# Performance work log

Hardware: AMD Instinct MI355X
Metric: run time of the kernel (lower is better)

The kernel has to match this reference:

```python
import math
import jax, jax.numpy as jnp
import numpy as np

B, T, C = 4, 2048, 1024
H = 16
D = C // H  # head dim = 64


def setup_inputs() -> dict:
    key = jax.random.key(0)
    ks = jax.random.split(key, 9)
    s = 0.02
    return {
        "x": jax.random.normal(ks[0], (B, T, C), dtype=jnp.float32),
        "Wq": jax.random.normal(ks[1], (C, C), dtype=jnp.float32) * s,
        "bq": jax.random.normal(ks[2], (C,), dtype=jnp.float32) * s,
        "Wk": jax.random.normal(ks[3], (C, C), dtype=jnp.float32) * s,
        "bk": jax.random.normal(ks[4], (C,), dtype=jnp.float32) * s,
        "Wv": jax.random.normal(ks[5], (C, C), dtype=jnp.float32) * s,
        "bv": jax.random.normal(ks[6], (C,), dtype=jnp.float32) * s,
        "Wo": jax.random.normal(ks[7], (C, C), dtype=jnp.float32) * s,
        "bo": jax.random.normal(ks[8], (C,), dtype=jnp.float32) * s,
    }


def reference(x, Wq, bq, Wk, bk, Wv, bv, Wo, bo):
    # Linear projections (torch Linear: x @ W.T + b), split into heads -> [B,H,T,D]
    def heads(y):
        return y.reshape(B, T, H, D).transpose(0, 2, 1, 3)

    q = heads(x @ Wq.T + bq)
    k = heads(x @ Wk.T + bk)
    v = heads(x @ Wv.T + bv)

    # Full [B,H,T,T] score matrix, scaled by 1/sqrt(D) (no mask, dropout=0 / eval)
    scores = jnp.einsum("bhqd,bhkd->bhqk", q, k) / math.sqrt(D)
    attn = jax.nn.softmax(scores, axis=-1)
    out = jnp.einsum("bhqk,bhkd->bhqd", attn, v)
    out = out.transpose(0, 2, 1, 3).reshape(B, T, C)
    return out @ Wo.T + bo
```

## Files before the change

kernel.cpp:

```cpp
#include <hip/hip_runtime.h>
#include <hip/hip_bf16.h>
#include <stdint.h>

#define Bb 4
#define Tt 2048
#define Cc 1024
#define Hh 16
#define Dd 64

using bf16x8 = __bf16 __attribute__((ext_vector_type(8)));
using f32x4  = float  __attribute__((ext_vector_type(4)));
using f32x16 = float  __attribute__((ext_vector_type(16)));
typedef unsigned short u16;
typedef unsigned int   u32;

#if defined(__has_builtin) && __has_builtin(__builtin_amdgcn_exp2f)
#define EXP2F(x) __builtin_amdgcn_exp2f(x)
#else
#define EXP2F(x) exp2f(x)
#endif

#if defined(__has_builtin) && __has_builtin(__builtin_amdgcn_permlane32_swap)
#define PERMLANE32_SWAP(a, b)                                          \
  do {                                                                 \
    auto _r = __builtin_amdgcn_permlane32_swap((a), (b), false, false);\
    (a) = _r[0]; (b) = _r[1];                                          \
  } while (0)
#else
#define PERMLANE32_SWAP(a, b) \
  asm volatile("v_permlane32_swap_b32 %0, %1" : "+v"(a), "+v"(b))
#endif

__device__ __forceinline__ u16 f32_to_bf16(float f) {
  union { float f; unsigned u; } v; v.f = f;
  unsigned r = v.u + 0x7fffu + ((v.u >> 16) & 1u);
  return (u16)(r >> 16);
}

__device__ __forceinline__ void gl2lds16(const u16* g, u16* l) {
  __builtin_amdgcn_global_load_lds(
      (const __attribute__((address_space(1))) u32*)g,
      (__attribute__((address_space(3))) u32*)l, 16, 0, 0);
}

__global__ void cast_f32_to_bf16(const float* __restrict__ in, u16* __restrict__ out, int n) {
  int i = (blockIdx.x * blockDim.x + threadIdx.x) * 4;
  if (i >= n) return;
  float4 v = *reinterpret_cast<const float4*>(in + i);
  ushort4 o;
  o.x = f32_to_bf16(v.x); o.y = f32_to_bf16(v.y);
  o.z = f32_to_bf16(v.z); o.w = f32_to_bf16(v.w);
  *reinterpret_cast<ushort4*>(out + i) = o;
}

__global__ void cast4_f32_to_bf16(const float* __restrict__ w0, const float* __restrict__ w1,
                                  const float* __restrict__ w2, const float* __restrict__ w3,
                                  u16* __restrict__ o0, u16* __restrict__ o1,
                                  u16* __restrict__ o2, u16* __restrict__ o3, int n) {
  const float* in; u16* out;
  switch (blockIdx.y) {
    case 0: in = w0; out = o0; break;
    case 1: in = w1; out = o1; break;
    case 2: in = w2; out = o2; break;
    default: in = w3; out = o3; break;
  }
  int i = (blockIdx.x * blockDim.x + threadIdx.x) * 4;
  if (i >= n) return;
  float4 v = *reinterpret_cast<const float4*>(in + i);
  ushort4 o;
  o.x = f32_to_bf16(v.x); o.y = f32_to_bf16(v.y);
  o.z = f32_to_bf16(v.z); o.w = f32_to_bf16(v.w);
  *reinterpret_cast<ushort4*>(out + i) = o;
}

__global__ __launch_bounds__(256, 2)
void gemm_qkv(const u16* __restrict__ A, const u16* __restrict__ Bqkv,
              const float* __restrict__ bq, const float* __restrict__ bk,
              const float* __restrict__ bv,
              u16* __restrict__ qout, u16* __restrict__ kout, u16* __restrict__ vtout,
              float qscl)
{
  constexpr int K = Cc, BK = 32, LDT = 136;
  __shared__ alignas(16) u16 smem[128 * LDT];
  u16* As = smem;
  u16* Bs = smem + 128 * BK;
  const int tid  = threadIdx.x;
  const int wave = tid >> 6, lane = tid & 63;
  const int row0 = blockIdx.x * 128, col0 = blockIdx.y * 128;
  const int seg  = col0 >> 10;
  const int wm = (wave & 1) * 64, wn = (wave >> 1) * 64;
  const int fr = lane & 15, fk = (lane >> 4) * 8;
  const int srow = lane >> 2, scol = (lane & 3) * 8;

  f32x4 acc[4][4] = {};

  for (int k0 = 0; k0 < K; k0 += BK) {
#pragma unroll
    for (int c = 0; c < 2; ++c) {
      int rg = (wave * 2 + c) * 16;
      gl2lds16(A    + (size_t)(row0 + rg + srow) * K + k0 + scol, &As[rg * BK]);
      gl2lds16(Bqkv + (size_t)(col0 + rg + srow) * K + k0 + scol, &Bs[rg * BK]);
    }
    __syncthreads();
    bf16x8 af[4], bf[4];
#pragma unroll
    for (int i = 0; i < 4; ++i) {
      af[i] = *reinterpret_cast<const bf16x8*>(&As[(wm + i * 16 + fr) * BK + fk]);
      bf[i] = *reinterpret_cast<const bf16x8*>(&Bs[(wn + i * 16 + fr) * BK + fk]);
    }
#pragma unroll
    for (int i = 0; i < 4; ++i)
#pragma unroll
      for (int j = 0; j < 4; ++j)
        acc[i][j] = __builtin_amdgcn_mfma_f32_16x16x32_bf16(af[i], bf[j], acc[i][j], 0, 0, 0);
    __syncthreads();
  }

  const float* bias = (seg == 0) ? bq : ((seg == 1) ? bk : bv);
  const float scale = (seg == 0) ? qscl : 1.0f;
  const int colL0 = col0 & 1023;

  if (seg < 2) {
    u16* outp = (seg == 0) ? qout : kout;
#pragma unroll
    for (int j = 0; j < 4; ++j) {
      int col = colL0 + wn + j * 16 + fr;
      float bvv = bias[col];
#pragma unroll
      for (int i = 0; i < 4; ++i) {
        int rowb = row0 + wm + i * 16 + (lane >> 4) * 4;
#pragma unroll
        for (int r = 0; r < 4; ++r)
          outp[(size_t)(rowb + r) * Cc + col] = f32_to_bf16((acc[i][j][r] + bvv) * scale);
      }
    }
  } else {
#pragma unroll
    for (int j = 0; j < 4; ++j) {
      int lc = wn + j * 16 + fr;
      float bvv = bias[colL0 + lc];
#pragma unroll
      for (int i = 0; i < 4; ++i) {
        int lr = wm + i * 16 + (lane >> 4) * 4;
#pragma unroll
        for (int r = 0; r < 4; ++r)
          smem[lc * LDT + lr + r] = f32_to_bf16(acc[i][j][r] + bvv);
      }
    }
    __syncthreads();
    int lc = tid >> 1, seg2 = tid & 1;
    int col = colL0 + lc;
    int h = col >> 6, d = col & 63;
    int bb = row0 >> 11, t0 = (row0 & 2047) + seg2 * 64;
    u16* dst = vtout + ((size_t)(bb * Hh + h) * Dd + d) * Tt + t0;
    const u16* src = &smem[lc * LDT + seg2 * 64];
#pragma unroll
    for (int g = 0; g < 8; ++g)
      *reinterpret_cast<uint4*>(dst + g * 8) = *reinterpret_cast<const uint4*>(src + g * 8);
  }
}

__global__ __launch_bounds__(256, 2)
void gemm_out(const u16* __restrict__ A, const u16* __restrict__ Bw,
              const float* __restrict__ bias, float* __restrict__ Cout,
              int M, int N, int K)
{
  constexpr int BK = 32;
  __shared__ alignas(16) u16 As[128 * BK];
  __shared__ alignas(16) u16 Bs[128 * BK];
  const int tid  = threadIdx.x;
  const int wave = tid >> 6, lane = tid & 63;
  const int row0 = blockIdx.x * 128, col0 = blockIdx.y * 128;
  const int wm = (wave & 1) * 64, wn = (wave >> 1) * 64;
  const int fr = lane & 15, fk = (lane >> 4) * 8;
  const int srow = lane >> 2, scol = (lane & 3) * 8;

  f32x4 acc[4][4] = {};

  for (int k0 = 0; k0 < K; k0 += BK) {
#pragma unroll
    for (int c = 0; c < 2; ++c) {
      int rg = (wave * 2 + c) * 16;
      gl2lds16(A  + (size_t)(row0 + rg + srow) * K + k0 + scol, &As[rg * BK]);
      gl2lds16(Bw + (size_t)(col0 + rg + srow) * K + k0 + scol, &Bs[rg * BK]);
    }
    __syncthreads();
    bf16x8 af[4], bf[4];
#pragma unroll
    for (int i = 0; i < 4; ++i) {
      af[i] = *reinterpret_cast<const bf16x8*>(&As[(wm + i * 16 + fr) * BK + fk]);
      bf[i] = *reinterpret_cast<const bf16x8*>(&Bs[(wn + i * 16 + fr) * BK + fk]);
    }
#pragma unroll
    for (int i = 0; i < 4; ++i)
#pragma unroll
      for (int j = 0; j < 4; ++j)
        acc[i][j] = __builtin_amdgcn_mfma_f32_16x16x32_bf16(af[i], bf[j], acc[i][j], 0, 0, 0);
    __syncthreads();
  }

#pragma unroll
  for (int j = 0; j < 4; ++j) {
    int col = col0 + wn + j * 16 + fr;
    float bv = bias[col];
#pragma unroll
    for (int i = 0; i < 4; ++i) {
      int rowb = row0 + wm + i * 16 + (lane >> 4) * 4;
#pragma unroll
      for (int r = 0; r < 4; ++r)
        Cout[(size_t)(rowb + r) * N + col] = acc[i][j][r] + bv;
    }
  }
}

__global__ __launch_bounds__(256, 2)
void attn_kernel(const u16* __restrict__ Q, const u16* __restrict__ Kmat,
                 const u16* __restrict__ VT, u16* __restrict__ O) {
  __shared__ alignas(16) unsigned char smem[32768];
  u16* Ks = (u16*)smem;
  u16* Vs = (u16*)(smem + 16384);
  float* OfT = (float*)smem;
  float* Qs  = (float*)(smem + 17408);

  const int tid = threadIdx.x, wave = tid >> 6, lane = tid & 63;
  const int l31 = lane & 31, hi = lane >> 5;
  const int bh = blockIdx.x, qt0 = blockIdx.y;
  const int b = bh >> 4, h = bh & 15;
  const size_t base = (size_t)b * Tt * Cc + (size_t)h * Dd;
  const size_t vtb = (size_t)bh * Dd * Tt;

  bf16x8 qb[2][4];
#pragma unroll
  for (int qt = 0; qt < 2; ++qt) {
    const u16* qp = Q + base + (size_t)(qt0 * 64 + qt * 32 + l31) * Cc + hi * 8;
#pragma unroll
    for (int c = 0; c < 4; ++c)
      qb[qt][c] = *reinterpret_cast<const bf16x8*>(qp + c * 16);
  }

  f32x16 Oacc[2][2] = {};
  float ssum[2] = {0.f, 0.f};

  const int skey = tid >> 1, sd0 = (tid & 1) * 32;
  const int svd = tid >> 2, svc = tid & 3;

  for (int kt = 0; kt < Tt; kt += 128) {
#pragma unroll
    for (int i = 0; i < 4; ++i) {
      int d0 = sd0 + i * 8;
      uint4 kv = *reinterpret_cast<const uint4*>(Kmat + base + (size_t)(kt + skey) * Cc + d0);
      *reinterpret_cast<uint4*>(&Ks[skey * 64 + (((d0 >> 3) ^ (skey & 7)) << 3)]) = kv;
      int c = svc + i * 4;
      uint4 vv = *reinterpret_cast<const uint4*>(VT + vtb + (size_t)svd * Tt + kt + c * 8);
      *reinterpret_cast<uint4*>(&Vs[svd * 128 + ((c ^ (svd & 15)) << 3)]) = vv;
    }
    __syncthreads();

    bf16x8 ka[4], vb[2][2];
    const int key = wave * 32 + l31;
#pragma unroll
    for (int c = 0; c < 4; ++c)
      ka[c] = *reinterpret_cast<const bf16x8*>(
          &Ks[key * 64 + ((((c << 1) + hi) ^ (key & 7)) << 3)]);
#pragma unroll
    for (int k0i = 0; k0i < 2; ++k0i)
#pragma unroll
      for (int dh = 0; dh < 2; ++dh) {
        int drow = dh * 32 + l31;
        int ch = wave * 4 + k0i * 2 + hi;
        vb[k0i][dh] = *reinterpret_cast<const bf16x8*>(
            &Vs[drow * 128 + ((ch ^ (drow & 15)) << 3)]);
      }

#pragma unroll
    for (int qt = 0; qt < 2; ++qt) {
      f32x16 s = {};
#pragma unroll
      for (int c = 0; c < 4; ++c)
        s = __builtin_amdgcn_mfma_f32_32x32x16_bf16(ka[c], qb[qt][c], s, 0, 0, 0);
      unsigned pk[8];
      float sm = 0.f;
#pragma unroll
      for (int i = 0; i < 8; ++i) {
        float p0 = EXP2F(s[2 * i]), p1 = EXP2F(s[2 * i + 1]);
        sm += p0 + p1;
        union { __hip_bfloat162 h2; unsigned u; } cv;
        cv.h2 = __float22bfloat162_rn(make_float2(p0, p1));
        pk[i] = cv.u;
      }
      ssum[qt] += sm;
      unsigned a0 = pk[0], a1 = pk[1], a2 = pk[2], a3 = pk[3];
      unsigned b0 = pk[4], b1 = pk[5], b2 = pk[6], b3 = pk[7];
      PERMLANE32_SWAP(a0, a2);
      PERMLANE32_SWAP(a1, a3);
      PERMLANE32_SWAP(b0, b2);
      PERMLANE32_SWAP(b1, b3);
      union { unsigned u[4]; bf16x8 v; } plo, phi;
      plo.u[0] = a0; plo.u[1] = a1; plo.u[2] = a2; plo.u[3] = a3;
      phi.u[0] = b0; phi.u[1] = b1; phi.u[2] = b2; phi.u[3] = b3;
      Oacc[qt][0] = __builtin_amdgcn_mfma_f32_32x32x16_bf16(plo.v, vb[0][0], Oacc[qt][0], 0, 0, 0);
      Oacc[qt][1] = __builtin_amdgcn_mfma_f32_32x32x16_bf16(plo.v, vb[0][1], Oacc[qt][1], 0, 0, 0);
      Oacc[qt][0] = __builtin_amdgcn_mfma_f32_32x32x16_bf16(phi.v, vb[1][0], Oacc[qt][0], 0, 0, 0);
      Oacc[qt][1] = __builtin_amdgcn_mfma_f32_32x32x16_bf16(phi.v, vb[1][1], Oacc[qt][1], 0, 0, 0);
    }
    __syncthreads();
  }

#pragma unroll
  for (int qt = 0; qt < 2; ++qt) {
    float s = ssum[qt];
    s += __shfl_xor(s, 32, 64);
    if (hi == 0) Qs[wave * 64 + qt * 32 + l31] = s;
  }

  for (int w = 0; w < 4; ++w) {
    if (wave == w) {
#pragma unroll
      for (int qt = 0; qt < 2; ++qt)
#pragma unroll
        for (int dh = 0; dh < 2; ++dh) {
          int d = dh * 32 + l31;
          float* rowp = &OfT[d * 68 + qt * 32 + hi * 4];
#pragma unroll
          for (int g = 0; g < 4; ++g) {
            f32x4 v;
            v[0] = Oacc[qt][dh][g * 4 + 0]; v[1] = Oacc[qt][dh][g * 4 + 1];
            v[2] = Oacc[qt][dh][g * 4 + 2]; v[3] = Oacc[qt][dh][g * 4 + 3];
            float* dst = rowp + g * 8;
            if (w == 0) *reinterpret_cast<f32x4*>(dst) = v;
            else {
              f32x4 old = *reinterpret_cast<const f32x4*>(dst);
              *reinterpret_cast<f32x4*>(dst) = old + v;
            }
          }
        }
    }
    __syncthreads();
  }

  {
    int q = tid >> 2, dg = tid & 3;
    float qtot = Qs[q] + Qs[64 + q] + Qs[128 + q] + Qs[192 + q];
    float linv = 1.0f / qtot;
    alignas(16) u16 tmp[16];
#pragma unroll
    for (int i = 0; i < 16; ++i)
      tmp[i] = f32_to_bf16(OfT[(dg * 16 + i) * 68 + q] * linv);
    u16* op = O + base + (size_t)(qt0 * 64 + q) * Cc + dg * 16;
    *reinterpret_cast<uint4*>(op)     = *reinterpret_cast<const uint4*>(tmp);
    *reinterpret_cast<uint4*>(op + 8) = *reinterpret_cast<const uint4*>(tmp + 8);
  }
}

extern "C" void kernel_launch(void* const* d_in, const int* in_sizes, int n_in,
                              void* d_out, int out_size, void* d_ws, size_t ws_size,
                              hipStream_t stream) {
  const float* x  = (const float*)d_in[0];
  const float* Wq = (const float*)d_in[1];
  const float* bq = (const float*)d_in[2];
  const float* Wk = (const float*)d_in[3];
  const float* bk = (const float*)d_in[4];
  const float* Wv = (const float*)d_in[5];
  const float* bv = (const float*)d_in[6];
  const float* Wo = (const float*)d_in[7];
  const float* bo = (const float*)d_in[8];

  const size_t NX = (size_t)Bb * Tt * Cc;
  const size_t NW = (size_t)Cc * Cc;

  u16* ws  = (u16*)d_ws;
  u16* xb  = ws;
  u16* wqb = ws + NX;
  u16* wkb = wqb + NW;
  u16* wvb = wkb + NW;
  u16* wob = wvb + NW;
  u16* qb  = wob + NW;
  u16* kb  = qb + NX;
  u16* vtb = kb + NX;
  u16* attnb = xb;

  cast_f32_to_bf16<<<(int)(NX / 4 / 256), 256, 0, stream>>>(x, xb, (int)NX);
  cast4_f32_to_bf16<<<dim3((unsigned)(NW / 4 / 256), 4), 256, 0, stream>>>(
      Wq, Wk, Wv, Wo, wqb, wkb, wvb, wob, (int)NW);

  const float QSCL = 0.125f * 1.44269504f;
  gemm_qkv<<<dim3(64, 24), 256, 0, stream>>>(xb, wqb, bq, bk, bv, qb, kb, vtb, QSCL);

  attn_kernel<<<dim3(Bb * Hh, Tt / 64), 256, 0, stream>>>(qb, kb, vtb, attnb);

  gemm_out<<<dim3(64, 8), 256, 0, stream>>>(attnb, wob, bo, (float*)d_out,
                                            Bb * Tt, Cc, Cc);
}
```

Measured before the change: 307.4 us.

## Double-buffer K/V tiles in LDS using direct global-to-LDS loads

Replaces the synchronous per-iteration K/V staging (global load to registers, then LDS store) with direct global-to-LDS copies into two 32KB buffers. The next tile is prefetched while the current one is consumed, so a barrier is needed only once per iteration. The aim is to hide global memory latency behind the MFMA work. In exchange the kernel uses 64KB of LDS, which may limit how many blocks fit per CU under launch_bounds(256,2). The swizzle layout is recomputed per lane to match the existing read pattern.

Result: no change. 307.3 us (-0.0%).

```diff
diff --git a/kernel.cpp b/kernel.cpp
--- a/kernel.cpp
+++ b/kernel.cpp
@@ -216,9 +216,7 @@
 __global__ __launch_bounds__(256, 2)
 void attn_kernel(const u16* __restrict__ Q, const u16* __restrict__ Kmat,
                  const u16* __restrict__ VT, u16* __restrict__ O) {
-  __shared__ alignas(16) unsigned char smem[32768];
-  u16* Ks = (u16*)smem;
-  u16* Vs = (u16*)(smem + 16384);
+  __shared__ alignas(16) unsigned char smem[65536];
   float* OfT = (float*)smem;
   float* Qs  = (float*)(smem + 17408);
 
@@ -241,20 +239,37 @@
   f32x16 Oacc[2][2] = {};
   float ssum[2] = {0.f, 0.f};
 
-  const int skey = tid >> 1, sd0 = (tid & 1) * 32;
-  const int svd = tid >> 2, svc = tid & 3;
-
-  for (int kt = 0; kt < Tt; kt += 128) {
-#pragma unroll
-    for (int i = 0; i < 4; ++i) {
-      int d0 = sd0 + i * 8;
-      uint4 kv = *reinterpret_cast<const uint4*>(Kmat + base + (size_t)(kt + skey) * Cc + d0);
-      *reinterpret_cast<uint4*>(&Ks[skey * 64 + (((d0 >> 3) ^ (skey & 7)) << 3)]) = kv;
-      int c = svc + i * 4;
-      uint4 vv = *reinterpret_cast<const uint4*>(VT + vtb + (size_t)svd * Tt + kt + c * 8);
-      *reinterpret_cast<uint4*>(&Vs[svd * 128 + ((c ^ (svd & 15)) << 3)]) = vv;
-    }
-    __syncthreads();
+  const u16* pK = Kmat + base + (size_t)(wave * 32 + (lane >> 3)) * Cc +
+                  (((lane & 7) ^ (lane >> 3)) << 3);
+  const u16* pV[4];
+#pragma unroll
+  for (int c = 0; c < 4; ++c) {
+    int d = wave * 16 + c * 4 + (lane >> 4);
+    int cs = (lane & 15) ^ ((c << 2) + (lane >> 4));
+    pV[c] = VT + vtb + (size_t)d * Tt + (cs << 3);
+  }
+
+  auto STAGE = [&](int buf, int kt) {
+    u16* Kd = (u16*)(smem + (buf << 15)) + wave * 2048;
+    u16* Vd = Kd + 8192;
+    const u16* pk = pK + (size_t)kt * Cc;
+#pragma unroll
+    for (int c = 0; c < 4; ++c) {
+      gl2lds16(pk + (size_t)(c * 8) * Cc, Kd + c * 512);
+      gl2lds16(pV[c] + kt, Vd + c * 512);
+    }
+  };
+
+  STAGE(0, 0);
+  __syncthreads();
+
+  int cur = 0;
+#pragma unroll 1
+  for (int t = 0; t < 16; ++t) {
+    if (t < 15) STAGE(cur ^ 1, (t + 1) << 7);
+
+    const u16* Ks = (const u16*)(smem + (cur << 15));
+    const u16* Vs = Ks + 8192;
 
     bf16x8 ka[4], vb[2][2];
     const int key = wave * 32 + l31;
@@ -278,7 +293,7 @@
 #pragma unroll
       for (int c = 0; c < 4; ++c)
         s = __builtin_amdgcn_mfma_f32_32x32x16_bf16(ka[c], qb[qt][c], s, 0, 0, 0);
-      unsigned pk[8];
+      unsigned pk8[8];
       float sm = 0.f;
 #pragma unroll
       for (int i = 0; i < 8; ++i) {
@@ -286,11 +301,11 @@
         sm += p0 + p1;
         union { __hip_bfloat162 h2; unsigned u; } cv;
         cv.h2 = __float22bfloat162_rn(make_float2(p0, p1));
-        pk[i] = cv.u;
+        pk8[i] = cv.u;
       }
       ssum[qt] += sm;
-      unsigned a0 = pk[0], a1 = pk[1], a2 = pk[2], a3 = pk[3];
-      unsigned b0 = pk[4], b1 = pk[5], b2 = pk[6], b3 = pk[7];
+      unsigned a0 = pk8[0], a1 = pk8[1], a2 = pk8[2], a3 = pk8[3];
+      unsigned b0 = pk8[4], b1 = pk8[5], b2 = pk8[6], b3 = pk8[7];
       PERMLANE32_SWAP(a0, a2);
       PERMLANE32_SWAP(a1, a3);
       PERMLANE32_SWAP(b0, b2);
@@ -304,6 +319,7 @@
       Oacc[qt][1] = __builtin_amdgcn_mfma_f32_32x32x16_bf16(phi.v, vb[1][1], Oacc[qt][1], 0, 0, 0);
     }
     __syncthreads();
+    cur ^= 1;
   }
 
 #pragma unroll
```
